# Kernel tuning notes

Hardware: AMD Instinct MI355X
Metric: run time of the kernel (lower is better)

## Reference

```python
import jax, jax.numpy as jnp
import numpy as np

D_MODEL = 1024
NUM_HEADS = 16
D_K = D_MODEL // NUM_HEADS


def setup_inputs() -> dict:
    key = jax.random.key(0)
    ks = jax.random.split(key, 9)
    s = 1.0 / np.sqrt(D_MODEL)
    x = jax.random.normal(ks[0], (4, 2048, D_MODEL), dtype=jnp.float32)
    Wq = jax.random.uniform(ks[1], (D_MODEL, D_MODEL), jnp.float32, -s, s)
    bq = jax.random.uniform(ks[2], (D_MODEL,), jnp.float32, -s, s)
    Wk = jax.random.uniform(ks[3], (D_MODEL, D_MODEL), jnp.float32, -s, s)
    bk = jax.random.uniform(ks[4], (D_MODEL,), jnp.float32, -s, s)
    Wv = jax.random.uniform(ks[5], (D_MODEL, D_MODEL), jnp.float32, -s, s)
    bv = jax.random.uniform(ks[6], (D_MODEL,), jnp.float32, -s, s)
    Wo = jax.random.uniform(ks[7], (D_MODEL, D_MODEL), jnp.float32, -s, s)
    bo = jax.random.uniform(ks[8], (D_MODEL,), jnp.float32, -s, s)
    return {"x": x, "Wq": Wq, "bq": bq, "Wk": Wk, "bk": bk,
            "Wv": Wv, "bv": bv, "Wo": Wo, "bo": bo}


def reference(x, Wq, bq, Wk, bk, Wv, bv, Wo, bo):
    B, T, C = x.shape
    H, Dk = NUM_HEADS, D_K
    # linear projections (torch Linear: x @ W.T + b; here W stored as [in,out])
    q = (x @ Wq + bq).reshape(B, T, H, Dk).transpose(0, 2, 1, 3)  # [B,H,T,Dk]
    k = (x @ Wk + bk).reshape(B, T, H, Dk).transpose(0, 2, 1, 3)
    v = (x @ Wv + bv).reshape(B, T, H, Dk).transpose(0, 2, 1, 3)
    scores = jnp.einsum("bhtd,bhsd->bhts", q, k) / jnp.sqrt(jnp.float32(Dk))
    attn = jax.nn.softmax(scores, axis=-1)  # [B,H,T,T]
    context = jnp.einsum("bhts,bhsd->bhtd", attn, v)
    context = context.transpose(0, 2, 1, 3).reshape(B, T, C)
    return context @ Wo + bo
```

## Files before the change

### kernel.cpp

```cpp
#include <hip/hip_runtime.h>
#include <hip/hip_bf16.h>
#include <stdint.h>

typedef short bf16x8 __attribute__((ext_vector_type(8)));
typedef short bf16x4 __attribute__((ext_vector_type(4)));
typedef float f32x4  __attribute__((ext_vector_type(4)));

#define MFMA16(a, b, c) __builtin_amdgcn_mfma_f32_16x16x32_bf16((a), (b), (c), 0, 0, 0)

__device__ __forceinline__ unsigned short f2bf(float f) {
    union { float f; unsigned int u; } v; v.f = f;
    unsigned int u = v.u;
    u += 0x7fffu + ((u >> 16) & 1u);
    return (unsigned short)(u >> 16);
}

__device__ __forceinline__ unsigned int trunc_pk(float a, float b) {
    return (__float_as_uint(a) >> 16) | (__float_as_uint(b) & 0xffff0000u);
}

__device__ __forceinline__ float exp2f_fast(float x) {
#if __has_builtin(__builtin_amdgcn_exp2f)
    return __builtin_amdgcn_exp2f(x);
#else
    return exp2f(x);
#endif
}

__device__ __forceinline__ void g2lds16(const void* g, void* l) {
    __builtin_amdgcn_global_load_lds(
        (const __attribute__((address_space(1))) void*)g,
        (__attribute__((address_space(3))) void*)l, 16, 0, 0);
}


__global__ __launch_bounds__(256) void prep_kernel(
    const float4* __restrict__ src, ushort4* __restrict__ dst,
    const float* __restrict__ W0, const float* __restrict__ W1,
    const float* __restrict__ W2, const float* __restrict__ W3,
    unsigned short* __restrict__ wdst_base)
{
    __shared__ float tile[64][65];
    const int id = blockIdx.x;
    if (id < 8192) {
        int i = id * 256 + threadIdx.x;
        float4 v = src[i];
        ushort4 o;
        o.x = f2bf(v.x); o.y = f2bf(v.y); o.z = f2bf(v.z); o.w = f2bf(v.w);
        dst[i] = o;
    } else {
        const int r = id - 8192;
        const int z = r >> 8, rem = r & 255;
        const float* wsrc = (z == 0) ? W0 : (z == 1) ? W1 : (z == 2) ? W2 : W3;
        unsigned short* wdst = wdst_base + ((size_t)z << 20);
        const int k0 = (rem & 15) * 64, n0 = (rem >> 4) * 64;
        const int tx = threadIdx.x & 63, ty = threadIdx.x >> 6;
        #pragma unroll
        for (int i = 0; i < 64; i += 4)
            tile[ty + i][tx] = wsrc[(size_t)(k0 + ty + i) * 1024 + n0 + tx];
        __syncthreads();
        #pragma unroll
        for (int i = 0; i < 64; i += 4)
            wdst[(size_t)(n0 + ty + i) * 1024 + k0 + tx] = f2bf(tile[tx][ty + i]);
    }
}


#define QSCALE 0.18033688011112042f

template <int MODE>
__global__ __launch_bounds__(512, 2) void gemm256(
    const unsigned short* __restrict__ A, const unsigned short* __restrict__ Bt,
    const float* __restrict__ b0, const float* __restrict__ b1, const float* __restrict__ b2,
    unsigned short* __restrict__ Qb, unsigned short* __restrict__ Kb,
    unsigned short* __restrict__ Vt, float* __restrict__ out)
{
    __shared__ alignas(16) unsigned short As[3][256 * 64];
    __shared__ alignas(16) unsigned short Bs[3][128 * 64];

    const int t = threadIdx.x;
    const int m0 = blockIdx.y * 256, n0 = blockIdx.x * 128;
    const int lane = t & 63, w = t >> 6, quad = lane >> 4, c16 = lane & 15;
    const int moff = (w >> 1) * 64;
    const int noff = (w & 1) * 64;

    f32x4 acc[4][4];
    #pragma unroll
    for (int i = 0; i < 4; ++i)
        #pragma unroll
        for (int j = 0; j < 4; ++j)
            acc[i][j] = (f32x4){0.f, 0.f, 0.f, 0.f};

    const int sg = (t & 7) ^ ((t >> 3) & 7);
    const unsigned short* Agl = A  + (size_t)(m0 + (t >> 3)) * 1024 + sg * 8;
    const unsigned short* Bgl = Bt + (size_t)(n0 + (t >> 3)) * 1024 + sg * 8;
    const int tOff = t * 8;

    const unsigned short *pA0 = &As[0][0], *pA1 = &As[1][0], *pA2 = &As[2][0];
    const unsigned short *pB0 = &Bs[0][0], *pB1 = &Bs[1][0], *pB2 = &Bs[2][0];

#define STAGE(Ad, Bd, k0v)                                                  \
    do {                                                                    \
        unsigned short* Adp = (unsigned short*)(Ad) + tOff;                 \
        unsigned short* Bdp = (unsigned short*)(Bd) + tOff;                 \
        g2lds16(Agl + (k0v),              Adp);                             \
        g2lds16(Agl + (k0v) + 65536,      Adp + 4096);                      \
        g2lds16(Agl + (k0v) + 2 * 65536,  Adp + 2 * 4096);                  \
        g2lds16(Agl + (k0v) + 3 * 65536,  Adp + 3 * 4096);                  \
        g2lds16(Bgl + (k0v),              Bdp);                             \
        g2lds16(Bgl + (k0v) + 65536,      Bdp + 4096);                      \
    } while (0)

    STAGE(pA0, pB0, 0);
    STAGE(pA1, pB1, 64);

    const int swz = c16 & 7;

    for (int kt = 0; kt < 16; ++kt) {
        if (kt < 15) {
            asm volatile("s_waitcnt vmcnt(6)" ::: "memory");
        } else {
            asm volatile("s_waitcnt vmcnt(0)" ::: "memory");
        }
        __builtin_amdgcn_sched_barrier(0);
        __builtin_amdgcn_s_barrier();
        __builtin_amdgcn_sched_barrier(0);

        #pragma unroll
        for (int kh = 0; kh < 2; ++kh) {
            const int fgr = ((kh * 4 + quad) ^ swz) << 3;
            bf16x8 af[4], bfr[4];
            #pragma unroll
            for (int ms = 0; ms < 4; ++ms)
                af[ms] = *(const bf16x8*)(pA0 + (moff + ms * 16 + c16) * 64 + fgr);
            #pragma unroll
            for (int ns = 0; ns < 4; ++ns)
                bfr[ns] = *(const bf16x8*)(pB0 + (noff + ns * 16 + c16) * 64 + fgr);

            if (kh == 0 && kt < 14)
                STAGE(pA2, pB2, (size_t)(kt + 2) * 64);

            asm volatile("s_waitcnt lgkmcnt(0)" ::: "memory");
            __builtin_amdgcn_sched_barrier(0);

            __builtin_amdgcn_s_setprio(1);
            #pragma unroll
            for (int ms = 0; ms < 4; ++ms)
                #pragma unroll
                for (int ns = 0; ns < 4; ++ns)
                    acc[ms][ns] = MFMA16(af[ms], bfr[ns], acc[ms][ns]);
            __builtin_amdgcn_s_setprio(0);

            if (kh == 0) {
                __builtin_amdgcn_sched_barrier(0);
                __builtin_amdgcn_s_barrier();
                __builtin_amdgcn_sched_barrier(0);
            }
        }

        const unsigned short* ta = pA0; pA0 = pA1; pA1 = pA2; pA2 = ta;
        const unsigned short* tb = pB0; pB0 = pB1; pB1 = pB2; pB2 = tb;
    }
#undef STAGE

    #pragma unroll
    for (int ns = 0; ns < 4; ++ns) {
        const int n = n0 + noff + ns * 16 + c16;
        if (MODE == 0) {
            const int mat = n >> 10, nn = n & 1023;
            const int h = nn >> 6, d = nn & 63;
            const float bias = (mat == 0) ? b0[nn] : ((mat == 1) ? b1[nn] : b2[nn]);
            #pragma unroll
            for (int ms = 0; ms < 4; ++ms) {
                const int mbase = m0 + moff + ms * 16 + quad * 4;
                const int b = mbase >> 11, tbase = mbase & 2047;
                const int bh = b * 16 + h;
                if (mat == 2) {
                    ushort4 pk;
                    pk.x = f2bf(acc[ms][ns][0] + bias);
                    pk.y = f2bf(acc[ms][ns][1] + bias);
                    pk.z = f2bf(acc[ms][ns][2] + bias);
                    pk.w = f2bf(acc[ms][ns][3] + bias);
                    *(ushort4*)(Vt + ((size_t)bh * 64 + d) * 2048 + tbase) = pk;
                } else {
                    #pragma unroll
                    for (int r = 0; r < 4; ++r) {
                        float v = acc[ms][ns][r] + bias;
                        if (mat == 0) v *= QSCALE;
                        unsigned short* dst = (mat == 0) ? Qb : Kb;
                        dst[((size_t)bh * 2048 + tbase + r) * 64 + d] = f2bf(v);
                    }
                }
            }
        } else {
            const float bias = b0[n];
            #pragma unroll
            for (int ms = 0; ms < 4; ++ms) {
                #pragma unroll
                for (int r = 0; r < 4; ++r) {
                    const int m = m0 + moff + ms * 16 + quad * 4 + r;
                    out[(size_t)m * 1024 + n] = acc[ms][ns][r] + bias;
                }
            }
        }
    }
}


__global__ __launch_bounds__(256, 4) void attn_kernel(
    const unsigned short* __restrict__ Qb, const unsigned short* __restrict__ Kb,
    const unsigned short* __restrict__ Vt, unsigned short* __restrict__ ctx)
{
    __shared__ alignas(16) unsigned short Ks[2][64 * 64];
    __shared__ alignas(16) unsigned short Vs[2][64 * 64];

    const int t = threadIdx.x, w = t >> 6, lane = t & 63;
    const int quad = lane >> 4, c16 = lane & 15;
    const int L = blockIdx.y * 16 + blockIdx.x;
    const int bh = ((L & 7) << 3) + (L >> 7);
    const int qt = (L >> 3) & 15;
    const int qbase = qt * 128 + w * 32;

    bf16x8 qf[2][2];
    #pragma unroll
    for (int mt = 0; mt < 2; ++mt) {
        const unsigned short* Qp = Qb + ((size_t)bh * 2048 + qbase + mt * 16 + c16) * 64;
        qf[mt][0] = *(const bf16x8*)(Qp + quad * 8);
        qf[mt][1] = *(const bf16x8*)(Qp + 32 + quad * 8);
    }

    float l_r[2] = {0.f, 0.f};
    f32x4 O[2][4];
    #pragma unroll
    for (int mt = 0; mt < 2; ++mt)
        #pragma unroll
        for (int dc = 0; dc < 4; ++dc) O[mt][dc] = (f32x4){0.f, 0.f, 0.f, 0.f};

    const int sgrp = (t & 7) ^ ((t >> 3) & 7);
    const unsigned short* Kgl = Kb + (size_t)bh * 131072 + (size_t)(t >> 3) * 64 + sgrp * 8;
    const unsigned short* Vgl = Vt + (size_t)bh * 131072 + (size_t)(t >> 3) * 2048 + sgrp * 8;
    const int tOff = t * 8;
    const f32x4 fzero = {0.f, 0.f, 0.f, 0.f};

    #pragma unroll
    for (int q = 0; q < 2; ++q) {
        g2lds16(Kgl + q * 2048,  Ks[0] + tOff + q * 2048);
        g2lds16(Vgl + (size_t)q * 65536, Vs[0] + tOff + q * 2048);
    }

    for (int it = 0; it < 32; ++it) {
        const int cur = it & 1;
        const unsigned short* Kc = Ks[cur];
        const unsigned short* Vc = Vs[cur];

        if (it < 31) {
            const int s0 = (it + 1) * 64;
            unsigned short* Kn = Ks[cur ^ 1] + tOff;
            unsigned short* Vn = Vs[cur ^ 1] + tOff;
            #pragma unroll
            for (int q = 0; q < 2; ++q) {
                g2lds16(Kgl + (size_t)s0 * 64 + q * 2048,    Kn + q * 2048);
                g2lds16(Vgl + s0 + (size_t)q * 65536,        Vn + q * 2048);
            }
            asm volatile("s_waitcnt vmcnt(4)" ::: "memory");
        } else {
            asm volatile("s_waitcnt vmcnt(0)" ::: "memory");
        }
        __builtin_amdgcn_sched_barrier(0);
        __builtin_amdgcn_s_barrier();
        __builtin_amdgcn_sched_barrier(0);

        #pragma unroll
        for (int ctp = 0; ctp < 2; ++ctp) {
            union { bf16x8 v; unsigned int d[4]; } af8[2];
            union { bf16x8 v; uint2 u[2]; } v8[4];

            #pragma unroll
            for (int ct2 = 0; ct2 < 2; ++ct2) {
                const int ct = ctp * 2 + ct2;
                const int key = ct * 16 + c16;
                const bf16x8 kf0 = *(const bf16x8*)(Kc + key * 64 + ((quad ^ (key & 7)) << 3));
                const bf16x8 kf1 = *(const bf16x8*)(Kc + key * 64 + (((4 + quad) ^ (key & 7)) << 3));

                const int g = ct * 2 + (quad >> 1);
                #pragma unroll
                for (int dc = 0; dc < 4; ++dc) {
                    const int d = dc * 16 + c16;
                    v8[dc].u[ct2] = *(const uint2*)(Vc + d * 64 + ((g ^ (d & 7)) << 3) + (quad & 1) * 4);
                }

                #pragma unroll
                for (int mt = 0; mt < 2; ++mt) {
                    f32x4 sa = MFMA16(kf0, qf[mt][0], fzero);
                    sa = MFMA16(kf1, qf[mt][1], sa);
                    const float p0 = exp2f_fast(sa[0]);
                    const float p1 = exp2f_fast(sa[1]);
                    const float p2 = exp2f_fast(sa[2]);
                    const float p3 = exp2f_fast(sa[3]);
                    l_r[mt] += (p0 + p1) + (p2 + p3);
                    af8[mt].d[ct2 * 2 + 0] = trunc_pk(p0, p1);
                    af8[mt].d[ct2 * 2 + 1] = trunc_pk(p2, p3);
                }
            }

            #pragma unroll
            for (int mt = 0; mt < 2; ++mt)
                #pragma unroll
                for (int dc = 0; dc < 4; ++dc)
                    O[mt][dc] = MFMA16(af8[mt].v, v8[dc].v, O[mt][dc]);
        }

        if (it < 31) {
            asm volatile("s_waitcnt lgkmcnt(0)" ::: "memory");
            __builtin_amdgcn_sched_barrier(0);
            __builtin_amdgcn_s_barrier();
            __builtin_amdgcn_sched_barrier(0);
        }
    }

    #pragma unroll
    for (int mt = 0; mt < 2; ++mt) {
        l_r[mt] += __shfl_xor(l_r[mt], 16);
        l_r[mt] += __shfl_xor(l_r[mt], 32);
    }

    const int b = bh >> 4, h = bh & 15;
    #pragma unroll
    for (int mt = 0; mt < 2; ++mt) {
        float inv[4];
        #pragma unroll
        for (int r = 0; r < 4; ++r)
            inv[r] = 1.0f / __shfl(l_r[mt], quad * 4 + r);
        #pragma unroll
        for (int dc = 0; dc < 4; ++dc)
            #pragma unroll
            for (int r = 0; r < 4; ++r) {
                const int row = qbase + mt * 16 + quad * 4 + r;
                ctx[((size_t)(b * 2048 + row)) * 1024 + h * 64 + dc * 16 + c16] =
                    f2bf(O[mt][dc][r] * inv[r]);
            }
    }
}


extern "C" void kernel_launch(void* const* d_in, const int* in_sizes, int n_in,
                              void* d_out, int out_size, void* d_ws, size_t ws_size,
                              hipStream_t stream)
{
    const float* x  = (const float*)d_in[0];
    const float* Wq = (const float*)d_in[1];
    const float* bq = (const float*)d_in[2];
    const float* Wk = (const float*)d_in[3];
    const float* bk = (const float*)d_in[4];
    const float* Wv = (const float*)d_in[5];
    const float* bv = (const float*)d_in[6];
    const float* Wo = (const float*)d_in[7];
    const float* bo = (const float*)d_in[8];
    float* out = (float*)d_out;

    char* ws = (char*)d_ws;
    unsigned short* xb    = (unsigned short*)(ws);
    unsigned short* Wqkvt = (unsigned short*)(ws + (16u << 20));
    unsigned short* Vt    = (unsigned short*)(ws + (24u << 20));
    unsigned short* Wot   = Wqkvt + (3u << 20);
    unsigned short* Qb    = (unsigned short*)((char*)d_out);
    unsigned short* Kb    = (unsigned short*)((char*)d_out + (16u << 20));

    prep_kernel<<<9216, 256, 0, stream>>>((const float4*)x, (ushort4*)xb,
                                          Wq, Wk, Wv, Wo, Wqkvt);

    gemm256<0><<<dim3(24, 32), 512, 0, stream>>>(xb, Wqkvt, bq, bk, bv, Qb, Kb, Vt, nullptr);
    attn_kernel<<<dim3(16, 64), 256, 0, stream>>>(Qb, Kb, Vt, xb );
    gemm256<1><<<dim3(8, 32), 512, 0, stream>>>(xb, Wot, bo, nullptr, nullptr,
                                                nullptr, nullptr, nullptr, out);
}
```

Measured before the change: 271.2 us.

## Shrink projection GEMM tiles to 128x128x32 with 256-thread blocks

Replaces the 256x128x64 tile, 512-thread GEMM with a 128x128 tile, 32-wide K step and 4 waves, doubling the grid size. It drops the XOR swizzle of shared-memory rows, the half-step barrier and the setprio hints, and issues the next prefetch before reading fragments. The aim is more blocks per CU and simpler scheduling, at the cost of less data reuse per tile, more K iterations, and possible LDS bank conflicts now that the swizzle is gone.

```diff
diff --git a/kernel.cpp b/kernel.cpp
--- a/kernel.cpp
+++ b/kernel.cpp
@@ -69,20 +69,19 @@
 #define QSCALE 0.18033688011112042f
 
 template <int MODE>
-__global__ __launch_bounds__(512, 2) void gemm256(
+__global__ __launch_bounds__(256, 3) void gemm_bt(
     const unsigned short* __restrict__ A, const unsigned short* __restrict__ Bt,
     const float* __restrict__ b0, const float* __restrict__ b1, const float* __restrict__ b2,
     unsigned short* __restrict__ Qb, unsigned short* __restrict__ Kb,
     unsigned short* __restrict__ Vt, float* __restrict__ out)
 {
-    __shared__ alignas(16) unsigned short As[3][256 * 64];
-    __shared__ alignas(16) unsigned short Bs[3][128 * 64];
+    __shared__ alignas(16) unsigned short As[3][128 * 32];
+    __shared__ alignas(16) unsigned short Bs[3][128 * 32];
 
     const int t = threadIdx.x;
-    const int m0 = blockIdx.y * 256, n0 = blockIdx.x * 128;
+    const int m0 = blockIdx.y * 128, n0 = blockIdx.x * 128;
     const int lane = t & 63, w = t >> 6, quad = lane >> 4, c16 = lane & 15;
-    const int moff = (w >> 1) * 64;
-    const int noff = (w & 1) * 64;
+    const int moff = (w >> 1) * 64, noff = (w & 1) * 64;
 
     f32x4 acc[4][4];
     #pragma unroll
@@ -91,75 +90,53 @@
         for (int j = 0; j < 4; ++j)
             acc[i][j] = (f32x4){0.f, 0.f, 0.f, 0.f};
 
-    const int sg = (t & 7) ^ ((t >> 3) & 7);
-    const unsigned short* Agl = A  + (size_t)(m0 + (t >> 3)) * 1024 + sg * 8;
-    const unsigned short* Bgl = Bt + (size_t)(n0 + (t >> 3)) * 1024 + sg * 8;
+    const unsigned short* Ag = A + (size_t)(m0 + (t >> 2)) * 1024 + (t & 3) * 8;
+    const unsigned short* Bg = Bt + (size_t)(n0 + (t >> 2)) * 1024 + (t & 3) * 8;
     const int tOff = t * 8;
 
-    const unsigned short *pA0 = &As[0][0], *pA1 = &As[1][0], *pA2 = &As[2][0];
-    const unsigned short *pB0 = &Bs[0][0], *pB1 = &Bs[1][0], *pB2 = &Bs[2][0];
+    unsigned short *pA0 = &As[0][0], *pA1 = &As[1][0], *pA2 = &As[2][0];
+    unsigned short *pB0 = &Bs[0][0], *pB1 = &Bs[1][0], *pB2 = &Bs[2][0];
 
 #define STAGE(Ad, Bd, k0v)                                                  \
     do {                                                                    \
-        unsigned short* Adp = (unsigned short*)(Ad) + tOff;                 \
-        unsigned short* Bdp = (unsigned short*)(Bd) + tOff;                 \
-        g2lds16(Agl + (k0v),              Adp);                             \
-        g2lds16(Agl + (k0v) + 65536,      Adp + 4096);                      \
-        g2lds16(Agl + (k0v) + 2 * 65536,  Adp + 2 * 4096);                  \
-        g2lds16(Agl + (k0v) + 3 * 65536,  Adp + 3 * 4096);                  \
-        g2lds16(Bgl + (k0v),              Bdp);                             \
-        g2lds16(Bgl + (k0v) + 65536,      Bdp + 4096);                      \
+        g2lds16(Ag + (k0v),             (Ad) + tOff);                       \
+        g2lds16(Ag + 65536 + (k0v),     (Ad) + tOff + 2048);                \
+        g2lds16(Bg + (k0v),             (Bd) + tOff);                       \
+        g2lds16(Bg + 65536 + (k0v),     (Bd) + tOff + 2048);                \
     } while (0)
 
     STAGE(pA0, pB0, 0);
-    STAGE(pA1, pB1, 64);
-
-    const int swz = c16 & 7;
-
-    for (int kt = 0; kt < 16; ++kt) {
-        if (kt < 15) {
-            asm volatile("s_waitcnt vmcnt(6)" ::: "memory");
+    STAGE(pA1, pB1, 32);
+
+    for (int kt = 0; kt < 32; ++kt) {
+        if (kt < 31) {
+            asm volatile("s_waitcnt vmcnt(4)" ::: "memory");
         } else {
             asm volatile("s_waitcnt vmcnt(0)" ::: "memory");
         }
-        __builtin_amdgcn_sched_barrier(0);
         __builtin_amdgcn_s_barrier();
         __builtin_amdgcn_sched_barrier(0);
 
-        #pragma unroll
-        for (int kh = 0; kh < 2; ++kh) {
-            const int fgr = ((kh * 4 + quad) ^ swz) << 3;
-            bf16x8 af[4], bfr[4];
-            #pragma unroll
-            for (int ms = 0; ms < 4; ++ms)
-                af[ms] = *(const bf16x8*)(pA0 + (moff + ms * 16 + c16) * 64 + fgr);
+        if (kt < 30)
+            STAGE(pA2, pB2, (kt + 2) * 32);
+
+        bf16x8 af[4], bfr[4];
+        #pragma unroll
+        for (int ms = 0; ms < 4; ++ms)
+            af[ms] = *(const bf16x8*)(pA0 + (moff + ms * 16 + c16) * 32 + quad * 8);
+        #pragma unroll
+        for (int ns = 0; ns < 4; ++ns)
+            bfr[ns] = *(const bf16x8*)(pB0 + (noff + ns * 16 + c16) * 32 + quad * 8);
+        #pragma unroll
+        for (int ms = 0; ms < 4; ++ms)
             #pragma unroll
             for (int ns = 0; ns < 4; ++ns)
-                bfr[ns] = *(const bf16x8*)(pB0 + (noff + ns * 16 + c16) * 64 + fgr);
-
-            if (kh == 0 && kt < 14)
-                STAGE(pA2, pB2, (size_t)(kt + 2) * 64);
-
-            asm volatile("s_waitcnt lgkmcnt(0)" ::: "memory");
-            __builtin_amdgcn_sched_barrier(0);
-
-            __builtin_amdgcn_s_setprio(1);
-            #pragma unroll
-            for (int ms = 0; ms < 4; ++ms)
-                #pragma unroll
-                for (int ns = 0; ns < 4; ++ns)
-                    acc[ms][ns] = MFMA16(af[ms], bfr[ns], acc[ms][ns]);
-            __builtin_amdgcn_s_setprio(0);
-
-            if (kh == 0) {
-                __builtin_amdgcn_sched_barrier(0);
-                __builtin_amdgcn_s_barrier();
-                __builtin_amdgcn_sched_barrier(0);
-            }
-        }
-
-        const unsigned short* ta = pA0; pA0 = pA1; pA1 = pA2; pA2 = ta;
-        const unsigned short* tb = pB0; pB0 = pB1; pB1 = pB2; pB2 = tb;
+                acc[ms][ns] = MFMA16(af[ms], bfr[ns], acc[ms][ns]);
+
+        __builtin_amdgcn_sched_barrier(0);
+
+        unsigned short* ta = pA0; pA0 = pA1; pA1 = pA2; pA2 = ta;
+        unsigned short* tb = pB0; pB0 = pB1; pB1 = pB2; pB2 = tb;
     }
 #undef STAGE
 
@@ -369,8 +346,8 @@
     prep_kernel<<<9216, 256, 0, stream>>>((const float4*)x, (ushort4*)xb,
                                           Wq, Wk, Wv, Wo, Wqkvt);
 
-    gemm256<0><<<dim3(24, 32), 512, 0, stream>>>(xb, Wqkvt, bq, bk, bv, Qb, Kb, Vt, nullptr);
+    gemm_bt<0><<<dim3(24, 64), 256, 0, stream>>>(xb, Wqkvt, bq, bk, bv, Qb, Kb, Vt, nullptr);
     attn_kernel<<<dim3(16, 64), 256, 0, stream>>>(Qb, Kb, Vt, xb );
-    gemm256<1><<<dim3(8, 32), 512, 0, stream>>>(xb, Wot, bo, nullptr, nullptr,
+    gemm_bt<1><<<dim3(8, 64), 256, 0, stream>>>(xb, Wot, bo, nullptr, nullptr,
                                                 nullptr, nullptr, nullptr, out);
 }
```

Result: slower. 282.3 us (+4.1%).
